# Kernel tuning notes

Measured on AMD Instinct MI355X. Metric: run time of the kernel, lower is better.

Reference implementation:

```python
import jax, jax.numpy as jnp
import numpy as np

N = 100000      # nodes (cells)
E = 1600000     # edges (kNN graph, avg degree 16)
DIM_IN = 128    # input features per cell
H = 8           # heads
C1 = 8          # per-head channels, layer 1 (concat -> 64)
DIM_OUT = 10    # classes (concat=False -> mean over heads)
NEG_SLOPE = 0.2


def setup_inputs() -> dict:
    key = jax.random.key(0)
    ks = jax.random.split(key, 10)
    s = 0.1
    return {
        "x": jax.random.normal(ks[0], (N, DIM_IN), dtype=jnp.float32),
        "edge_index": jax.random.randint(ks[1], (2, E), 0, N, dtype=jnp.int64),
        "W1": jax.random.normal(ks[2], (DIM_IN, H * C1), dtype=jnp.float32) * s,
        "a_src1": jax.random.normal(ks[3], (H, C1), dtype=jnp.float32) * s,
        "a_dst1": jax.random.normal(ks[4], (H, C1), dtype=jnp.float32) * s,
        "b1": jnp.zeros((H * C1,), dtype=jnp.float32),
        "W2": jax.random.normal(ks[5], (H * C1, H * DIM_OUT), dtype=jnp.float32) * s,
        "a_src2": jax.random.normal(ks[6], (H, DIM_OUT), dtype=jnp.float32) * s,
        "a_dst2": jax.random.normal(ks[7], (H, DIM_OUT), dtype=jnp.float32) * s,
        "b2": jnp.zeros((DIM_OUT,), dtype=jnp.float32),
    }


def _gat_layer(x, src, dst, W, a_src, a_dst, bias, concat, n):
    """PyG-style GATConv: gather -> edge attention -> segment softmax -> scatter."""
    h_, c_ = a_src.shape
    h = (x @ W).reshape(n, h_, c_)                       # [N, H, C]
    alpha_s = jnp.einsum('nhc,hc->nh', h, a_src)         # [N, H]
    alpha_d = jnp.einsum('nhc,hc->nh', h, a_dst)         # [N, H]
    # per-edge logits; PyG: message from src j to dst i, softmax over dst
    e = jax.nn.leaky_relu(alpha_s[src] + alpha_d[dst], NEG_SLOPE)  # [E, H]
    e_max = jax.ops.segment_max(e, dst, num_segments=n)            # [N, H]
    e = jnp.exp(e - e_max[dst])
    denom = jax.ops.segment_sum(e, dst, num_segments=n)            # [N, H]
    alpha = e / denom[dst]                                          # [E, H]
    msg = h[src] * alpha[:, :, None]                                # [E, H, C]
    out = jax.ops.segment_sum(msg, dst, num_segments=n)             # [N, H, C]
    out = out.reshape(n, h_ * c_) if concat else out.mean(axis=1)
    return out + bias


def reference(x, edge_index, W1, a_src1, a_dst1, b1, W2, a_src2, a_dst2, b2):
    n = x.shape[0]
    loops = jnp.arange(n, dtype=edge_index.dtype)
    src = jnp.concatenate([edge_index[0], loops])  # PyG adds self-loops by default
    dst = jnp.concatenate([edge_index[1], loops])
    h = _gat_layer(x, src, dst, W1, a_src1, a_dst1, b1, True, n)   # [N, 64]
    h = jax.nn.elu(h)
    h = _gat_layer(h, src, dst, W2, a_src2, a_dst2, b2, False, n)  # [N, dim_out]
    return jax.nn.log_softmax(h, axis=1)
```

## Files before the change

kernel.cpp:

```cpp
#include <hip/hip_runtime.h>
#include <hip/hip_bf16.h>
#include <cstdint>

#define CAP 64
#define SLICES 8
#define CHUNK_EDGES 2048

__device__ __forceinline__ float lrelu(float v) { return fmaxf(v, 0.2f * v); }

typedef float f32x2 __attribute__((ext_vector_type(2)));
__device__ __forceinline__ float2 q2f(unsigned short u) {
    f32x2 v = __builtin_amdgcn_cvt_pk_f32_fp8((int)u, false);
    return make_float2(v.x, v.y);
}
__device__ __forceinline__ int f2q4(float a, float b, float c, float d) {
    int p = __builtin_amdgcn_cvt_pk_fp8_f32(a, b, 0, false);
    p = __builtin_amdgcn_cvt_pk_fp8_f32(c, d, p, true);
    return p;
}
__device__ __forceinline__ float b2f(unsigned short u) { return __uint_as_float(((unsigned)u) << 16); }
__device__ __forceinline__ unsigned short f2b(float f) {
    unsigned u = __float_as_uint(f);
    return (unsigned short)((u + 0x7FFFu + ((u >> 16) & 1u)) >> 16);
}

__global__ __launch_bounds__(256, 4) void k_bg(const int* __restrict__ ei, int E, int N,
                                               int* __restrict__ cnt, int* __restrict__ bucket,
                                               const float* __restrict__ x,
                                               const float* __restrict__ W,
                                               const float* __restrict__ asrc,
                                               const float* __restrict__ adst,
                                               unsigned char* __restrict__ h1q,
                                               float* __restrict__ als, float* __restrict__ ald,
                                               int buildBlocks) {
    __shared__ unsigned short xs[64 * 132];
    if ((int)blockIdx.x < buildBlocks) {
        const int s = blockIdx.x & (SLICES - 1);
        const int chunk = blockIdx.x >> 3;
        const int sliceN = (N + SLICES - 1) / SLICES;
        const int lo = s * sliceN;
        const int hi = min(N, lo + sliceN);
        const int base = chunk * CHUNK_EDGES;
        if (base + CHUNK_EDGES <= E) {
            const int e0 = base + (int)threadIdx.x * 4;
            const int e1 = e0 + 1024;
            int4 d0 = *(const int4*)(ei + E + e0);
            int4 s0 = *(const int4*)(ei + e0);
            int4 d1 = *(const int4*)(ei + E + e1);
            int4 s1 = *(const int4*)(ei + e1);
            int a0 = -1, a1 = -1, a2 = -1, a3 = -1, a4 = -1, a5 = -1, a6 = -1, a7 = -1;
            if (d0.x >= lo && d0.x < hi) a0 = atomicAdd(&cnt[d0.x], 1);
            if (d0.y >= lo && d0.y < hi) a1 = atomicAdd(&cnt[d0.y], 1);
            if (d0.z >= lo && d0.z < hi) a2 = atomicAdd(&cnt[d0.z], 1);
            if (d0.w >= lo && d0.w < hi) a3 = atomicAdd(&cnt[d0.w], 1);
            if (d1.x >= lo && d1.x < hi) a4 = atomicAdd(&cnt[d1.x], 1);
            if (d1.y >= lo && d1.y < hi) a5 = atomicAdd(&cnt[d1.y], 1);
            if (d1.z >= lo && d1.z < hi) a6 = atomicAdd(&cnt[d1.z], 1);
            if (d1.w >= lo && d1.w < hi) a7 = atomicAdd(&cnt[d1.w], 1);
            if (a0 >= 0 && a0 < CAP) bucket[(size_t)d0.x * CAP + a0] = s0.x;
            if (a1 >= 0 && a1 < CAP) bucket[(size_t)d0.y * CAP + a1] = s0.y;
            if (a2 >= 0 && a2 < CAP) bucket[(size_t)d0.z * CAP + a2] = s0.z;
            if (a3 >= 0 && a3 < CAP) bucket[(size_t)d0.w * CAP + a3] = s0.w;
            if (a4 >= 0 && a4 < CAP) bucket[(size_t)d1.x * CAP + a4] = s1.x;
            if (a5 >= 0 && a5 < CAP) bucket[(size_t)d1.y * CAP + a5] = s1.y;
            if (a6 >= 0 && a6 < CAP) bucket[(size_t)d1.z * CAP + a6] = s1.z;
            if (a7 >= 0 && a7 < CAP) bucket[(size_t)d1.w * CAP + a7] = s1.w;
        } else {
            const int end = E;
            for (int e = base + (int)threadIdx.x; e < end; e += 256) {
                int d = ei[E + e];
                if (d >= lo && d < hi) {
                    int a = atomicAdd(&cnt[d], 1);
                    if (a < CAP) bucket[(size_t)d * CAP + a] = ei[e];
                }
            }
        }
        return;
    }
    const int t = threadIdx.x;
    const int rowBase = ((int)blockIdx.x - buildBlocks) * 64;
#pragma unroll
    for (int i = 0; i < 8; ++i) {
        int g = i * 256 + t;
        int r = g >> 5, c4 = (g & 31) << 2;
        float4 v = make_float4(0.f, 0.f, 0.f, 0.f);
        int row = rowBase + r;
        if (row < N) v = *(const float4*)(x + (size_t)row * 128 + c4);
        ushort4 u;
        u.x = f2b(v.x); u.y = f2b(v.y); u.z = f2b(v.z); u.w = f2b(v.w);
        *(ushort4*)(&xs[r * 132 + c4]) = u;
    }
    __syncthreads();
    const int tx = t & 15;
    const int ty = t >> 4;
    float acc[4][4] = {};
#pragma unroll 2
    for (int kc = 0; kc < 32; ++kc) {
        float a_[4][4];
#pragma unroll
        for (int i = 0; i < 4; ++i) {
            ushort4 u = *(const ushort4*)(&xs[(4 * ty + i) * 132 + kc * 4]);
            a_[i][0] = b2f(u.x); a_[i][1] = b2f(u.y); a_[i][2] = b2f(u.z); a_[i][3] = b2f(u.w);
        }
        float4 w[4];
#pragma unroll
        for (int kk = 0; kk < 4; ++kk) w[kk] = *(const float4*)(W + (size_t)(kc * 4 + kk) * 64 + tx * 4);
#pragma unroll
        for (int i = 0; i < 4; ++i) {
#pragma unroll
            for (int j = 0; j < 4; ++j) {
                acc[i][j] += a_[i][0] * ((const float*)&w[0])[j]
                           + a_[i][1] * ((const float*)&w[1])[j]
                           + a_[i][2] * ((const float*)&w[2])[j]
                           + a_[i][3] * ((const float*)&w[3])[j];
            }
        }
    }
    const int h = tx >> 1;
    float4 av = *(const float4*)(asrc + tx * 4);
    float4 dv = *(const float4*)(adst + tx * 4);
#pragma unroll
    for (int i = 0; i < 4; ++i) {
        int row = rowBase + 4 * ty + i;
        float ps = acc[i][0] * av.x + acc[i][1] * av.y + acc[i][2] * av.z + acc[i][3] * av.w;
        float pd = acc[i][0] * dv.x + acc[i][1] * dv.y + acc[i][2] * dv.z + acc[i][3] * dv.w;
        ps += __shfl_xor(ps, 1);
        pd += __shfl_xor(pd, 1);
        if (row < N) {
            *(int*)(h1q + (size_t)row * 64 + tx * 4) = f2q4(acc[i][0], acc[i][1], acc[i][2], acc[i][3]);
            if ((tx & 1) == 0) {
                als[(size_t)row * 8 + h] = ps;
                ald[(size_t)row * 8 + h] = pd;
            }
        }
    }
}

__global__ __launch_bounds__(256) void k_ag(const int* __restrict__ cnt, const int* __restrict__ bucket,
                                            const unsigned char* __restrict__ h1q,
                                            const float* __restrict__ als, const float* __restrict__ aldin,
                                            const float* __restrict__ b1,
                                            const float* __restrict__ W,
                                            const float* __restrict__ asrc,
                                            const float* __restrict__ adst,
                                            unsigned char* __restrict__ h2q,
                                            float* __restrict__ ald, int N) {
    __shared__ unsigned short xs[64 * 68];
    __shared__ unsigned short wt[80 * 68];
    const int t = threadIdx.x;
    const int rowBase = blockIdx.x * 64;
#pragma unroll
    for (int i = 0; i < 20; ++i) {
        int g = i * 256 + t;
        int k = g / 80, c = g % 80;
        wt[c * 68 + k] = f2b(W[g]);
    }
    {
        const int n = rowBase + (t >> 2);
        const int sub = t & 3;
        if (n < N) {
            float2 aldh = *(const float2*)(aldin + (size_t)n * 8 + sub * 2);
            float acc[16] = {};
            float den0 = 0.f, den1 = 0.f;
            auto body = [&](int4 m, float2 a_s, float val) {
                float wl0 = __expf(lrelu(a_s.x + aldh.x)) * val;
                float wl1 = __expf(lrelu(a_s.y + aldh.y)) * val;
                den0 += wl0; den1 += wl1;
                f32x2 v;
                v = __builtin_amdgcn_cvt_pk_f32_fp8(m.x, false); acc[0] += wl0 * v.x; acc[1] += wl0 * v.y;
                v = __builtin_amdgcn_cvt_pk_f32_fp8(m.x, true);  acc[2] += wl0 * v.x; acc[3] += wl0 * v.y;
                v = __builtin_amdgcn_cvt_pk_f32_fp8(m.y, false); acc[4] += wl0 * v.x; acc[5] += wl0 * v.y;
                v = __builtin_amdgcn_cvt_pk_f32_fp8(m.y, true);  acc[6] += wl0 * v.x; acc[7] += wl0 * v.y;
                v = __builtin_amdgcn_cvt_pk_f32_fp8(m.z, false); acc[8] += wl1 * v.x; acc[9] += wl1 * v.y;
                v = __builtin_amdgcn_cvt_pk_f32_fp8(m.z, true);  acc[10] += wl1 * v.x; acc[11] += wl1 * v.y;
                v = __builtin_amdgcn_cvt_pk_f32_fp8(m.w, false); acc[12] += wl1 * v.x; acc[13] += wl1 * v.y;
                v = __builtin_amdgcn_cvt_pk_f32_fp8(m.w, true);  acc[14] += wl1 * v.x; acc[15] += wl1 * v.y;
            };
            {
                body(*(const int4*)(h1q + (size_t)n * 64 + sub * 16),
                     *(const float2*)(als + (size_t)n * 8 + sub * 2), 1.f);
            }
            const int k = min(cnt[n], CAP);
            const int* bp = bucket + (size_t)n * CAP;
            if (k > 0) {
                const int kg = ((k - 1) >> 2) << 2;
                int4 nxt = *(const int4*)(bp);
                for (int i0 = 0; i0 < k; i0 += 4) {
                    int4 cur = nxt;
                    nxt = *(const int4*)(bp + min(i0 + 4, kg));
                    const int rem = k - i0;
                    const int s0 = cur.x;
                    const int s1 = (rem > 1) ? cur.y : cur.x;
                    const int s2 = (rem > 2) ? cur.z : cur.x;
                    const int s3 = (rem > 3) ? cur.w : cur.x;
                    const int4 r0 = *(const int4*)(h1q + (size_t)s0 * 64 + sub * 16);
                    const int4 r1 = *(const int4*)(h1q + (size_t)s1 * 64 + sub * 16);
                    const int4 r2 = *(const int4*)(h1q + (size_t)s2 * 64 + sub * 16);
                    const int4 r3 = *(const int4*)(h1q + (size_t)s3 * 64 + sub * 16);
                    const float2 a0 = *(const float2*)(als + (size_t)s0 * 8 + sub * 2);
                    const float2 a1 = *(const float2*)(als + (size_t)s1 * 8 + sub * 2);
                    const float2 a2 = *(const float2*)(als + (size_t)s2 * 8 + sub * 2);
                    const float2 a3 = *(const float2*)(als + (size_t)s3 * 8 + sub * 2);
                    body(r0, a0, 1.f);
                    body(r1, a1, (rem > 1) ? 1.f : 0.f);
                    body(r2, a2, (rem > 2) ? 1.f : 0.f);
                    body(r3, a3, (rem > 3) ? 1.f : 0.f);
                }
            }
            float inv0 = 1.f / den0, inv1 = 1.f / den1;
            const float* bb = b1 + sub * 16;
            float o[16];
#pragma unroll
            for (int j = 0; j < 8; ++j) {
                float v = acc[j] * inv0 + bb[j];
                o[j] = v > 0.f ? v : __expf(v) - 1.f;
            }
#pragma unroll
            for (int j = 8; j < 16; ++j) {
                float v = acc[j] * inv1 + bb[j];
                o[j] = v > 0.f ? v : __expf(v) - 1.f;
            }
            unsigned short* dst = &xs[(t >> 2) * 68 + sub * 16];
#pragma unroll
            for (int q = 0; q < 4; ++q) {
                ushort4 u;
                u.x = f2b(o[q * 4 + 0]); u.y = f2b(o[q * 4 + 1]);
                u.z = f2b(o[q * 4 + 2]); u.w = f2b(o[q * 4 + 3]);
                *(ushort4*)(dst + q * 4) = u;
            }
        }
    }
    __syncthreads();
    const int tx = t & 15;
    const int ty = t >> 4;
    float acc[4][5] = {};
#pragma unroll 4
    for (int kc = 0; kc < 16; ++kc) {
        float4 a[4];
#pragma unroll
        for (int i = 0; i < 4; ++i) {
            ushort4 u = *(const ushort4*)(&xs[(4 * ty + i) * 68 + kc * 4]);
            a[i] = make_float4(b2f(u.x), b2f(u.y), b2f(u.z), b2f(u.w));
        }
        float4 w[5];
#pragma unroll
        for (int j = 0; j < 5; ++j) {
            ushort4 u = *(const ushort4*)(&wt[(5 * tx + j) * 68 + kc * 4]);
            w[j] = make_float4(b2f(u.x), b2f(u.y), b2f(u.z), b2f(u.w));
        }
#pragma unroll
        for (int i = 0; i < 4; ++i) {
#pragma unroll
            for (int j = 0; j < 5; ++j) {
                acc[i][j] += a[i].x * w[j].x + a[i].y * w[j].y + a[i].z * w[j].z + a[i].w * w[j].w;
            }
        }
    }
    const int h = tx >> 1;
    float a2[5], d2[5];
#pragma unroll
    for (int j = 0; j < 5; ++j) { a2[j] = asrc[tx * 5 + j]; d2[j] = adst[tx * 5 + j]; }
    __syncthreads();
    unsigned char* qs = (unsigned char*)xs;
#pragma unroll
    for (int i = 0; i < 4; ++i) {
        int row = rowBase + 4 * ty + i;
        float ps = 0.f, pd = 0.f;
#pragma unroll
        for (int j = 0; j < 5; ++j) { ps += acc[i][j] * a2[j]; pd += acc[i][j] * d2[j]; }
        ps += __shfl_xor(ps, 1);
        pd += __shfl_xor(pd, 1);
        int p0 = __builtin_amdgcn_cvt_pk_fp8_f32(acc[i][0], acc[i][1], 0, false);
        int p1 = __builtin_amdgcn_cvt_pk_fp8_f32(acc[i][2], acc[i][3], 0, false);
        int p2 = __builtin_amdgcn_cvt_pk_fp8_f32(acc[i][4], acc[i][4], 0, false);
        unsigned char* q = qs + (4 * ty + i) * 96 + h * 12 + (tx & 1) * 5;
        q[0] = (unsigned char)(p0 & 0xFF);
        q[1] = (unsigned char)((p0 >> 8) & 0xFF);
        q[2] = (unsigned char)(p1 & 0xFF);
        q[3] = (unsigned char)((p1 >> 8) & 0xFF);
        q[4] = (unsigned char)(p2 & 0xFF);
        if ((tx & 1) == 0) {
            *(unsigned short*)(qs + (size_t)(4 * ty + i) * 96 + h * 12 + 10) = f2b(ps);
            if (row < N) ald[(size_t)row * 8 + h] = pd;
        }
    }
    __syncthreads();
    for (int g = t; g < 1536; g += 256) {
        int row = g / 24;
        if (rowBase + row < N)
            *(unsigned int*)(h2q + (size_t)rowBase * 96 + (size_t)g * 4) = ((unsigned int*)qs)[g];
    }
}

__global__ __launch_bounds__(256) void k_agg2(const int* __restrict__ cnt, const int* __restrict__ bucket,
                                              const unsigned char* __restrict__ h2q,
                                              const float* __restrict__ ald,
                                              const float* __restrict__ b2,
                                              float* __restrict__ out, int N) {
    const int t = threadIdx.x;
    const int n = blockIdx.x * 32 + (t >> 3);
    const int h = t & 7;
    if (n >= N) return;
    float acc[10] = {};
    float den = 0.f;
    const float aldh = ald[(size_t)n * 8 + h];
    auto body = [&](int m0, int m1, int m2, float val) {
        float a_s = b2f((unsigned short)(((unsigned)m2) >> 16));
        float wl = __expf(lrelu(a_s + aldh)) * val;
        den += wl;
        f32x2 v;
        v = __builtin_amdgcn_cvt_pk_f32_fp8(m0, false); acc[0] += wl * v.x; acc[1] += wl * v.y;
        v = __builtin_amdgcn_cvt_pk_f32_fp8(m0, true);  acc[2] += wl * v.x; acc[3] += wl * v.y;
        v = __builtin_amdgcn_cvt_pk_f32_fp8(m1, false); acc[4] += wl * v.x; acc[5] += wl * v.y;
        v = __builtin_amdgcn_cvt_pk_f32_fp8(m1, true);  acc[6] += wl * v.x; acc[7] += wl * v.y;
        v = __builtin_amdgcn_cvt_pk_f32_fp8(m2, false); acc[8] += wl * v.x; acc[9] += wl * v.y;
    };
    {
        const unsigned char* r = h2q + (size_t)n * 96 + h * 12;
        body(*(const int*)r, *(const int*)(r + 4), *(const int*)(r + 8), 1.f);
    }
    const int k = min(cnt[n], CAP);
    const int* bp = bucket + (size_t)n * CAP;
    if (k > 0) {
        const int kg4 = ((k - 1) >> 2) << 2;
        int4 lo = *(const int4*)(bp);
        int4 hi = *(const int4*)(bp + min(4, kg4));
        for (int i0 = 0; i0 < k; i0 += 8) {
            int4 cA = lo, cB = hi;
            lo = *(const int4*)(bp + min(i0 + 8, kg4));
            hi = *(const int4*)(bp + min(i0 + 12, kg4));
            const int rem = k - i0;
            int s[8];
            s[0] = cA.x;
            s[1] = (rem > 1) ? cA.y : cA.x;
            s[2] = (rem > 2) ? cA.z : cA.x;
            s[3] = (rem > 3) ? cA.w : cA.x;
            s[4] = (rem > 4) ? cB.x : cA.x;
            s[5] = (rem > 5) ? cB.y : cA.x;
            s[6] = (rem > 6) ? cB.z : cA.x;
            s[7] = (rem > 7) ? cB.w : cA.x;
            int m0[8], m1[8], m2[8];
#pragma unroll
            for (int j = 0; j < 8; ++j) {
                const unsigned char* p = h2q + (size_t)s[j] * 96 + h * 12;
                m0[j] = *(const int*)p;
                m1[j] = *(const int*)(p + 4);
                m2[j] = *(const int*)(p + 8);
            }
#pragma unroll
            for (int j = 0; j < 8; ++j) body(m0[j], m1[j], m2[j], (rem > j) ? 1.f : 0.f);
        }
    }
    float inv = 1.f / den;
#pragma unroll
    for (int j = 0; j < 10; ++j) acc[j] *= inv;
#pragma unroll
    for (int off = 1; off < 8; off <<= 1) {
#pragma unroll
        for (int j = 0; j < 10; ++j) acc[j] += __shfl_xor(acc[j], off);
    }
    if (h == 0) {
        float m[10];
#pragma unroll
        for (int j = 0; j < 10; ++j) m[j] = acc[j] * 0.125f + b2[j];
        float mx = -1e30f;
#pragma unroll
        for (int j = 0; j < 10; ++j) mx = fmaxf(mx, m[j]);
        float ssum = 0.f;
#pragma unroll
        for (int j = 0; j < 10; ++j) ssum += __expf(m[j] - mx);
        float lg = __logf(ssum);
#pragma unroll
        for (int j = 0; j < 10; ++j) out[(size_t)n * 10 + j] = m[j] - mx - lg;
    }
}

extern "C" void kernel_launch(void* const* d_in, const int* in_sizes, int n_in,
                              void* d_out, int out_size, void* d_ws, size_t ws_size,
                              hipStream_t stream) {
    const float* x     = (const float*)d_in[0];
    const int*   ei    = (const int*)d_in[1];
    const float* W1    = (const float*)d_in[2];
    const float* asrc1 = (const float*)d_in[3];
    const float* adst1 = (const float*)d_in[4];
    const float* b1    = (const float*)d_in[5];
    const float* W2    = (const float*)d_in[6];
    const float* asrc2 = (const float*)d_in[7];
    const float* adst2 = (const float*)d_in[8];
    const float* b2    = (const float*)d_in[9];
    float* out = (float*)d_out;

    int N = in_sizes[0] / 128;
    int E = in_sizes[1] / 2;

    char* base = (char*)d_ws;
    size_t off = 0;
    auto alloc = [&](size_t bytes) {
        char* p = base + off;
        off = (off + bytes + 255) & ~(size_t)255;
        return p;
    };
    int*            cnt    = (int*)alloc((size_t)N * 4);
    int*            bucket = (int*)alloc((size_t)N * CAP * 4);
    unsigned char*  h1q    = (unsigned char*)alloc((size_t)N * 64);
    unsigned char*  h2q    = (unsigned char*)alloc((size_t)N * 96);
    float*          als    = (float*)alloc((size_t)N * 8 * 4);
    float*          ald    = (float*)alloc((size_t)N * 8 * 4);
    (void)ws_size; (void)n_in; (void)out_size;

    (void)hipMemsetAsync(cnt, 0, (size_t)N * 4, stream);
    int chunks = (E + CHUNK_EDGES - 1) / CHUNK_EDGES;
    int buildBlocks = chunks * SLICES;
    int gemmBlocks = (N + 63) / 64;
    k_bg<<<buildBlocks + gemmBlocks, 256, 0, stream>>>(ei, E, N, cnt, bucket,
                                                       x, W1, asrc1, adst1, h1q, als, ald, buildBlocks);
    k_ag<<<(N + 63) / 64, 256, 0, stream>>>(cnt, bucket, h1q, als, ald, b1,
                                            W2, asrc2, adst2, h2q, ald, N);
    k_agg2<<<(N + 31) / 32, 256, 0, stream>>>(cnt, bucket, h2q, ald, b2, out, N);
}
```

Before: 310.5 us.

## Pack layer-1 source logits into per-head fp8 rows and remap aggregation threads

```diff
diff --git a/kernel.cpp b/kernel.cpp
--- a/kernel.cpp
+++ b/kernel.cpp
@@ -9,10 +9,6 @@
 __device__ __forceinline__ float lrelu(float v) { return fmaxf(v, 0.2f * v); }
 
 typedef float f32x2 __attribute__((ext_vector_type(2)));
-__device__ __forceinline__ float2 q2f(unsigned short u) {
-    f32x2 v = __builtin_amdgcn_cvt_pk_f32_fp8((int)u, false);
-    return make_float2(v.x, v.y);
-}
 __device__ __forceinline__ int f2q4(float a, float b, float c, float d) {
     int p = __builtin_amdgcn_cvt_pk_fp8_f32(a, b, 0, false);
     p = __builtin_amdgcn_cvt_pk_fp8_f32(c, d, p, true);
@@ -31,7 +27,7 @@
                                                const float* __restrict__ asrc,
                                                const float* __restrict__ adst,
                                                unsigned char* __restrict__ h1q,
-                                               float* __restrict__ als, float* __restrict__ ald,
+                                               float* __restrict__ ald,
                                                int buildBlocks) {
     __shared__ unsigned short xs[64 * 132];
     if ((int)blockIdx.x < buildBlocks) {
@@ -119,6 +115,8 @@
     const int h = tx >> 1;
     float4 av = *(const float4*)(asrc + tx * 4);
     float4 dv = *(const float4*)(adst + tx * 4);
+    __syncthreads();
+    unsigned char* qs = (unsigned char*)xs;
 #pragma unroll
     for (int i = 0; i < 4; ++i) {
         int row = rowBase + 4 * ty + i;
@@ -126,29 +124,34 @@
         float pd = acc[i][0] * dv.x + acc[i][1] * dv.y + acc[i][2] * dv.z + acc[i][3] * dv.w;
         ps += __shfl_xor(ps, 1);
         pd += __shfl_xor(pd, 1);
-        if (row < N) {
-            *(int*)(h1q + (size_t)row * 64 + tx * 4) = f2q4(acc[i][0], acc[i][1], acc[i][2], acc[i][3]);
-            if ((tx & 1) == 0) {
-                als[(size_t)row * 8 + h] = ps;
-                ald[(size_t)row * 8 + h] = pd;
-            }
-        }
+        *(int*)(qs + (4 * ty + i) * 96 + h * 12 + (tx & 1) * 4) =
+            f2q4(acc[i][0], acc[i][1], acc[i][2], acc[i][3]);
+        if ((tx & 1) == 0) {
+            *(unsigned short*)(qs + (4 * ty + i) * 96 + h * 12 + 8) = f2b(ps);
+            if (row < N) ald[(size_t)row * 8 + h] = pd;
+        }
+    }
+    __syncthreads();
+    for (int g = t; g < 1536; g += 256) {
+        int row = g / 24;
+        if (rowBase + row < N)
+            *(unsigned int*)(h1q + (size_t)rowBase * 96 + (size_t)g * 4) = ((unsigned int*)qs)[g];
     }
 }
 
 __global__ __launch_bounds__(256) void k_ag(const int* __restrict__ cnt, const int* __restrict__ bucket,
                                             const unsigned char* __restrict__ h1q,
-                                            const float* __restrict__ als, const float* __restrict__ aldin,
+                                            const float* __restrict__ aldin,
                                             const float* __restrict__ b1,
                                             const float* __restrict__ W,
                                             const float* __restrict__ asrc,
                                             const float* __restrict__ adst,
                                             unsigned char* __restrict__ h2q,
                                             float* __restrict__ ald, int N) {
-    __shared__ unsigned short xs[64 * 68];
+    __shared__ unsigned short xs[32 * 68];
     __shared__ unsigned short wt[80 * 68];
     const int t = threadIdx.x;
-    const int rowBase = blockIdx.x * 64;
+    const int rowBase = blockIdx.x * 32;
 #pragma unroll
     for (int i = 0; i < 20; ++i) {
         int g = i * 256 + t;
@@ -156,90 +159,84 @@
         wt[c * 68 + k] = f2b(W[g]);
     }
     {
-        const int n = rowBase + (t >> 2);
-        const int sub = t & 3;
+        const int nl = t >> 3;
+        const int h = t & 7;
+        const int n = rowBase + nl;
         if (n < N) {
-            float2 aldh = *(const float2*)(aldin + (size_t)n * 8 + sub * 2);
-            float acc[16] = {};
-            float den0 = 0.f, den1 = 0.f;
-            auto body = [&](int4 m, float2 a_s, float val) {
-                float wl0 = __expf(lrelu(a_s.x + aldh.x)) * val;
-                float wl1 = __expf(lrelu(a_s.y + aldh.y)) * val;
-                den0 += wl0; den1 += wl1;
+            const float aldh = aldin[(size_t)n * 8 + h];
+            float acc[8] = {};
+            float den = 0.f;
+            auto body = [&](int m0, int m1, int m2, float val) {
+                float a_s = b2f((unsigned short)(m2 & 0xFFFF));
+                float wl = __expf(lrelu(a_s + aldh)) * val;
+                den += wl;
                 f32x2 v;
-                v = __builtin_amdgcn_cvt_pk_f32_fp8(m.x, false); acc[0] += wl0 * v.x; acc[1] += wl0 * v.y;
-                v = __builtin_amdgcn_cvt_pk_f32_fp8(m.x, true);  acc[2] += wl0 * v.x; acc[3] += wl0 * v.y;
-                v = __builtin_amdgcn_cvt_pk_f32_fp8(m.y, false); acc[4] += wl0 * v.x; acc[5] += wl0 * v.y;
-                v = __builtin_amdgcn_cvt_pk_f32_fp8(m.y, true);  acc[6] += wl0 * v.x; acc[7] += wl0 * v.y;
-                v = __builtin_amdgcn_cvt_pk_f32_fp8(m.z, false); acc[8] += wl1 * v.x; acc[9] += wl1 * v.y;
-                v = __builtin_amdgcn_cvt_pk_f32_fp8(m.z, true);  acc[10] += wl1 * v.x; acc[11] += wl1 * v.y;
-                v = __builtin_amdgcn_cvt_pk_f32_fp8(m.w, false); acc[12] += wl1 * v.x; acc[13] += wl1 * v.y;
-                v = __builtin_amdgcn_cvt_pk_f32_fp8(m.w, true);  acc[14] += wl1 * v.x; acc[15] += wl1 * v.y;
+                v = __builtin_amdgcn_cvt_pk_f32_fp8(m0, false); acc[0] += wl * v.x; acc[1] += wl * v.y;
+                v = __builtin_amdgcn_cvt_pk_f32_fp8(m0, true);  acc[2] += wl * v.x; acc[3] += wl * v.y;
+                v = __builtin_amdgcn_cvt_pk_f32_fp8(m1, false); acc[4] += wl * v.x; acc[5] += wl * v.y;
+                v = __builtin_amdgcn_cvt_pk_f32_fp8(m1, true);  acc[6] += wl * v.x; acc[7] += wl * v.y;
             };
             {
-                body(*(const int4*)(h1q + (size_t)n * 64 + sub * 16),
-                     *(const float2*)(als + (size_t)n * 8 + sub * 2), 1.f);
+                const unsigned char* r = h1q + (size_t)n * 96 + h * 12;
+                body(*(const int*)r, *(const int*)(r + 4), *(const int*)(r + 8), 1.f);
             }
             const int k = min(cnt[n], CAP);
             const int* bp = bucket + (size_t)n * CAP;
             if (k > 0) {
-                const int kg = ((k - 1) >> 2) << 2;
-                int4 nxt = *(const int4*)(bp);
-                for (int i0 = 0; i0 < k; i0 += 4) {
-                    int4 cur = nxt;
-                    nxt = *(const int4*)(bp + min(i0 + 4, kg));
+                const int kg4 = ((k - 1) >> 2) << 2;
+                int4 lo = *(const int4*)(bp);
+                int4 hi = *(const int4*)(bp + min(4, kg4));
+                for (int i0 = 0; i0 < k; i0 += 8) {
+                    int4 cA = lo, cB = hi;
+                    lo = *(const int4*)(bp + min(i0 + 8, kg4));
+                    hi = *(const int4*)(bp + min(i0 + 12, kg4));
                     const int rem = k - i0;
-                    const int s0 = cur.x;
-                    const int s1 = (rem > 1) ? cur.y : cur.x;
-                    const int s2 = (rem > 2) ? cur.z : cur.x;
-                    const int s3 = (rem > 3) ? cur.w : cur.x;
-                    const int4 r0 = *(const int4*)(h1q + (size_t)s0 * 64 + sub * 16);
-                    const int4 r1 = *(const int4*)(h1q + (size_t)s1 * 64 + sub * 16);
-                    const int4 r2 = *(const int4*)(h1q + (size_t)s2 * 64 + sub * 16);
-                    const int4 r3 = *(const int4*)(h1q + (size_t)s3 * 64 + sub * 16);
-                    const float2 a0 = *(const float2*)(als + (size_t)s0 * 8 + sub * 2);
-                    const float2 a1 = *(const float2*)(als + (size_t)s1 * 8 + sub * 2);
-                    const float2 a2 = *(const float2*)(als + (size_t)s2 * 8 + sub * 2);
-                    const float2 a3 = *(const float2*)(als + (size_t)s3 * 8 + sub * 2);
-                    body(r0, a0, 1.f);
-                    body(r1, a1, (rem > 1) ? 1.f : 0.f);
-                    body(r2, a2, (rem > 2) ? 1.f : 0.f);
-                    body(r3, a3, (rem > 3) ? 1.f : 0.f);
+                    int s[8];
+                    s[0] = cA.x;
+                    s[1] = (rem > 1) ? cA.y : cA.x;
+                    s[2] = (rem > 2) ? cA.z : cA.x;
+                    s[3] = (rem > 3) ? cA.w : cA.x;
+                    s[4] = (rem > 4) ? cB.x : cA.x;
+                    s[5] = (rem > 5) ? cB.y : cA.x;
+                    s[6] = (rem > 6) ? cB.z : cA.x;
+                    s[7] = (rem > 7) ? cB.w : cA.x;
+                    int m0[8], m1[8], m2[8];
+#pragma unroll
+                    for (int j = 0; j < 8; ++j) {
+                        const unsigned char* p = h1q + (size_t)s[j] * 96 + h * 12;
+                        m0[j] = *(const int*)p;
+                        m1[j] = *(const int*)(p + 4);
+                        m2[j] = *(const int*)(p + 8);
+                    }
+#pragma unroll
+                    for (int j = 0; j < 8; ++j) body(m0[j], m1[j], m2[j], (rem > j) ? 1.f : 0.f);
                 }
             }
-            float inv0 = 1.f / den0, inv1 = 1.f / den1;
-            const float* bb = b1 + sub * 16;
-            float o[16];
+            float inv = 1.f / den;
+            float o[8];
 #pragma unroll
             for (int j = 0; j < 8; ++j) {
-                float v = acc[j] * inv0 + bb[j];
+                float v = acc[j] * inv + b1[h * 8 + j];
                 o[j] = v > 0.f ? v : __expf(v) - 1.f;
             }
-#pragma unroll
-            for (int j = 8; j < 16; ++j) {
-                float v = acc[j] * inv1 + bb[j];
-                o[j] = v > 0.f ? v : __expf(v) - 1.f;
-            }
-            unsigned short* dst = &xs[(t >> 2) * 68 + sub * 16];
-#pragma unroll
-            for (int q = 0; q < 4; ++q) {
-                ushort4 u;
-                u.x = f2b(o[q * 4 + 0]); u.y = f2b(o[q * 4 + 1]);
-                u.z = f2b(o[q * 4 + 2]); u.w = f2b(o[q * 4 + 3]);
-                *(ushort4*)(dst + q * 4) = u;
-            }
+            unsigned short* dst = &xs[nl * 68 + h * 8];
+            ushort4 u0, u1;
+            u0.x = f2b(o[0]); u0.y = f2b(o[1]); u0.z = f2b(o[2]); u0.w = f2b(o[3]);
+            u1.x = f2b(o[4]); u1.y = f2b(o[5]); u1.z = f2b(o[6]); u1.w = f2b(o[7]);
+            *(ushort4*)(dst) = u0;
+            *(ushort4*)(dst + 4) = u1;
         }
     }
     __syncthreads();
     const int tx = t & 15;
     const int ty = t >> 4;
-    float acc[4][5] = {};
+    float acc[2][5] = {};
 #pragma unroll 4
     for (int kc = 0; kc < 16; ++kc) {
-        float4 a[4];
-#pragma unroll
-        for (int i = 0; i < 4; ++i) {
-            ushort4 u = *(const ushort4*)(&xs[(4 * ty + i) * 68 + kc * 4]);
+        float4 a[2];
+#pragma unroll
+        for (int i = 0; i < 2; ++i) {
+            ushort4 u = *(const ushort4*)(&xs[(2 * ty + i) * 68 + kc * 4]);
             a[i] = make_float4(b2f(u.x), b2f(u.y), b2f(u.z), b2f(u.w));
         }
         float4 w[5];
@@ -249,7 +246,7 @@
             w[j] = make_float4(b2f(u.x), b2f(u.y), b2f(u.z), b2f(u.w));
         }
 #pragma unroll
-        for (int i = 0; i < 4; ++i) {
+        for (int i = 0; i < 2; ++i) {
 #pragma unroll
             for (int j = 0; j < 5; ++j) {
                 acc[i][j] += a[i].x * w[j].x + a[i].y * w[j].y + a[i].z * w[j].z + a[i].w * w[j].w;
@@ -263,8 +260,8 @@
     __syncthreads();
     unsigned char* qs = (unsigned char*)xs;
 #pragma unroll
-    for (int i = 0; i < 4; ++i) {
-        int row = rowBase + 4 * ty + i;
+    for (int i = 0; i < 2; ++i) {
+        int row = rowBase + 2 * ty + i;
         float ps = 0.f, pd = 0.f;
 #pragma unroll
         for (int j = 0; j < 5; ++j) { ps += acc[i][j] * a2[j]; pd += acc[i][j] * d2[j]; }
@@ -273,19 +270,19 @@
         int p0 = __builtin_amdgcn_cvt_pk_fp8_f32(acc[i][0], acc[i][1], 0, false);
         int p1 = __builtin_amdgcn_cvt_pk_fp8_f32(acc[i][2], acc[i][3], 0, false);
         int p2 = __builtin_amdgcn_cvt_pk_fp8_f32(acc[i][4], acc[i][4], 0, false);
-        unsigned char* q = qs + (4 * ty + i) * 96 + h * 12 + (tx & 1) * 5;
+        unsigned char* q = qs + (2 * ty + i) * 96 + h * 12 + (tx & 1) * 5;
         q[0] = (unsigned char)(p0 & 0xFF);
         q[1] = (unsigned char)((p0 >> 8) & 0xFF);
         q[2] = (unsigned char)(p1 & 0xFF);
         q[3] = (unsigned char)((p1 >> 8) & 0xFF);
         q[4] = (unsigned char)(p2 & 0xFF);
         if ((tx & 1) == 0) {
-            *(unsigned short*)(qs + (size_t)(4 * ty + i) * 96 + h * 12 + 10) = f2b(ps);
+            *(unsigned short*)(qs + (size_t)(2 * ty + i) * 96 + h * 12 + 10) = f2b(ps);
             if (row < N) ald[(size_t)row * 8 + h] = pd;
         }
     }
     __syncthreads();
-    for (int g = t; g < 1536; g += 256) {
+    for (int g = t; g < 768; g += 256) {
         int row = g / 24;
         if (rowBase + row < N)
             *(unsigned int*)(h2q + (size_t)rowBase * 96 + (size_t)g * 4) = ((unsigned int*)qs)[g];
@@ -402,9 +399,8 @@
     };
     int*            cnt    = (int*)alloc((size_t)N * 4);
     int*            bucket = (int*)alloc((size_t)N * CAP * 4);
-    unsigned char*  h1q    = (unsigned char*)alloc((size_t)N * 64);
+    unsigned char*  h1q    = (unsigned char*)alloc((size_t)N * 96);
     unsigned char*  h2q    = (unsigned char*)alloc((size_t)N * 96);
-    float*          als    = (float*)alloc((size_t)N * 8 * 4);
     float*          ald    = (float*)alloc((size_t)N * 8 * 4);
     (void)ws_size; (void)n_in; (void)out_size;
 
@@ -413,8 +409,8 @@
     int buildBlocks = chunks * SLICES;
     int gemmBlocks = (N + 63) / 64;
     k_bg<<<buildBlocks + gemmBlocks, 256, 0, stream>>>(ei, E, N, cnt, bucket,
-                                                       x, W1, asrc1, adst1, h1q, als, ald, buildBlocks);
-    k_ag<<<(N + 63) / 64, 256, 0, stream>>>(cnt, bucket, h1q, als, ald, b1,
+                                                       x, W1, asrc1, adst1, h1q, ald, buildBlocks);
+    k_ag<<<(N + 31) / 32, 256, 0, stream>>>(cnt, bucket, h1q, ald, b1,
                                             W2, asrc2, adst2, h2q, ald, N);
     k_agg2<<<(N + 31) / 32, 256, 0, stream>>>(cnt, bucket, h2q, ald, b2, out, N);
 }
```

Measured after the change: 298.4 us (median of 2 runs). 1.04x faster.
